# Performance work log

Measured on AMD Instinct MI355X. Metric: run time of the kernel, lower is better.

## Reference

```python
import jax, jax.numpy as jnp
import numpy as np

DIM_MODEL = 512
DIM_HEAD = 64


def setup_inputs() -> dict:
    key = jax.random.key(0)
    ks = jax.random.split(key, 7)
    B, S = 4, 4096
    x = jax.random.normal(ks[0], (B, S, DIM_MODEL), dtype=jnp.float32)
    mask = jnp.ones((B, 1, S), dtype=jnp.int32)
    # torch Linear init: U(-1/sqrt(fan_in), 1/sqrt(fan_in)); stored as (in, out) for x @ W
    bound = 1.0 / np.sqrt(DIM_MODEL)
    Wq = jax.random.uniform(ks[1], (DIM_MODEL, DIM_HEAD), minval=-bound, maxval=bound, dtype=jnp.float32)
    bq = jax.random.uniform(ks[2], (DIM_HEAD,), minval=-bound, maxval=bound, dtype=jnp.float32)
    Wk = jax.random.uniform(ks[3], (DIM_MODEL, DIM_HEAD), minval=-bound, maxval=bound, dtype=jnp.float32)
    bk = jax.random.uniform(ks[4], (DIM_HEAD,), minval=-bound, maxval=bound, dtype=jnp.float32)
    Wv = jax.random.uniform(ks[5], (DIM_MODEL, DIM_HEAD), minval=-bound, maxval=bound, dtype=jnp.float32)
    bv = jax.random.uniform(ks[6], (DIM_HEAD,), minval=-bound, maxval=bound, dtype=jnp.float32)
    return {"x": x, "mask": mask, "Wq": Wq, "bq": bq, "Wk": Wk, "bk": bk, "Wv": Wv, "bv": bv}


def reference(x, mask, Wq, bq, Wk, bk, Wv, bv):
    # single-head QKV projection
    q = x @ Wq + bq  # (B, S, Dh)
    k = x @ Wk + bk
    v = x @ Wv + bv
    dot_scale = jnp.sqrt(jnp.float32(DIM_HEAD))
    # explicit O(S^2) score matrix, softmax over keys
    scores = jnp.einsum("bqd,bkd->bqk", q, k) / dot_scale  # (B, S, S)
    attn = jax.nn.softmax(scores, axis=-1)
    # faithful to source: mask applied AFTER softmax with -inf fill
    attn = jnp.where(mask == 0, jnp.float32(-jnp.inf), attn)
    return jnp.einsum("bqk,bkd->bqd", attn, v)  # (B, S, Dh)
```

## Files before the change

kernel.cpp:

```cpp
#include <hip/hip_runtime.h>
#include <hip/hip_bf16.h>

typedef _Float16 half8v __attribute__((ext_vector_type(8)));
typedef _Float16 half4v __attribute__((ext_vector_type(4)));
typedef _Float16 half2v __attribute__((ext_vector_type(2)));
typedef __fp16   fp16x2 __attribute__((ext_vector_type(2)));
typedef __attribute__((ext_vector_type(4))) float floatx4;

#define LOG2E_OVER_8 0.18033688011112042f


__global__ __launch_bounds__(256) void wtrans_k(const float* __restrict__ Wq,
                                                const float* __restrict__ Wk,
                                                const float* __restrict__ Wv,
                                                _Float16* __restrict__ Wt) {
    int idx = blockIdx.x * 256 + threadIdx.x;
    int p = idx >> 15, rem = idx & 32767;
    int k = rem >> 6;
    int n = rem & 63;
    const float* W = (p == 0) ? Wq : ((p == 1) ? Wk : Wv);
    int ctg = p * 4 + (n >> 4), m = n & 15;
    int kc = k >> 5, quad = (k >> 3) & 3, j = k & 7;
    Wt[(((ctg << 4) + kc) * 64 + (quad << 4) + m) * 8 + j] = (_Float16)W[k * 64 + n];
}

#define XS_STRIDE 536
__global__ __launch_bounds__(256) void proj_k(const float* __restrict__ x,
                                              const _Float16* __restrict__ Wt,
                                              const float* __restrict__ bq,
                                              const float* __restrict__ bk,
                                              const float* __restrict__ bv,
                                              _Float16* __restrict__ Qh,
                                              _Float16* __restrict__ Kh,
                                              _Float16* __restrict__ Vh) {
    __shared__ _Float16 xs[16 * XS_STRIDE];

    int tid = threadIdx.x, l = tid & 63, wv = tid >> 6;
    int m = l & 15, quad = l >> 4;
    int row0 = blockIdx.x * 16;

#pragma unroll
    for (int i = 0; i < 8; i++) {
        int idx = tid + i * 256;
        int row = idx >> 7, c4 = idx & 127;
        float4 v = *(const float4*)(x + (row0 + row) * 512 + c4 * 4);
        union { half2v h[2]; uint2 u; } cv;
        cv.h[0][0] = (_Float16)v.x; cv.h[0][1] = (_Float16)v.y;
        cv.h[1][0] = (_Float16)v.z; cv.h[1][1] = (_Float16)v.w;
        *(uint2*)(xs + row * XS_STRIDE + c4 * 4) = cv.u;
    }
    __syncthreads();

    const _Float16* arow = xs + m * XS_STRIDE + quad * 8;

    floatx4 acc[3];
#pragma unroll
    for (int i = 0; i < 3; i++) acc[i] = (floatx4)(0.f);

#pragma unroll 4
    for (int kc = 0; kc < 16; kc++) {
        half8v a = *(const half8v*)(arow + kc * 32);
#pragma unroll
        for (int ct = 0; ct < 3; ct++) {
            int ctg = wv * 3 + ct;
            half8v b = *(const half8v*)(Wt + (((ctg << 4) + kc) * 64 + l) * 8);
            acc[ct] = __builtin_amdgcn_mfma_f32_16x16x32_f16(a, b, acc[ct], 0, 0, 0);
        }
    }

#pragma unroll
    for (int ct = 0; ct < 3; ct++) {
        int ctg = wv * 3 + ct;
        int col = ctg * 16 + m;
        float bias = (ctg < 4) ? bq[col] : ((ctg < 8) ? bk[col - 64] : bv[col - 128]);
        if (ctg < 8) {
            _Float16* dst = (ctg < 4) ? Qh : Kh;
            float scl = (ctg < 4) ? LOG2E_OVER_8 : 1.0f;
            int dd = (ctg & 3) * 16 + m;
            int c = dd >> 5, quadQ = (dd >> 3) & 3, j = dd & 7;
#pragma unroll
            for (int r = 0; r < 4; r++) {
                int row = row0 + quad * 4 + r;
                int chunk = ((row >> 4) << 1) + c;
                dst[(chunk * 64 + quadQ * 16 + (row & 15)) * 8 + j] =
                    (_Float16)((acc[ct][r] + bias) * scl);
            }
        } else {
            int dt = ctg - 8;
            int t64 = row0 >> 6, ktp = (row0 >> 5) & 1, half = (row0 >> 4) & 1;
            int chunk = t64 * 8 + dt * 2 + ktp;
            union { _Float16 h[4]; unsigned long long u; } pk;
#pragma unroll
            for (int r = 0; r < 4; r++) pk.h[r] = (_Float16)(acc[ct][r] + bias);
            *(unsigned long long*)(Vh + (chunk * 64 + quad * 16 + m) * 8 + half * 4) = pk.u;
        }
    }
}

__global__ __launch_bounds__(128) void attn_k(const _Float16* __restrict__ Qh,
                                              const _Float16* __restrict__ Kh,
                                              const _Float16* __restrict__ Vh,
                                              const int* __restrict__ mask,
                                              float* __restrict__ Np,
                                              float* __restrict__ Dp) {
    __shared__ __align__(16) uint4 buf[2][1024];

    int tid = threadIdx.x, l = tid & 63, wv = tid >> 6;
    int m = l & 15, quad = l >> 4;
    int bid = blockIdx.x;
    int qblk = bid >> 4, grp = bid & 15, os = grp >> 2, b = grp & 3;
    int q0 = qblk * 64 + wv * 32;

    const int* maskb = mask + b * 4096 + os * 1024;
    int az = 0;
#pragma unroll
    for (int i = 0; i < 16; i++) az |= (maskb[l + i * 64] == 0);
    const bool hasz = __any(az);

    int qt_g = (b * 4096 + q0) >> 4;
    half8v qf[2][2];
#pragma unroll
    for (int qt = 0; qt < 2; qt++)
#pragma unroll
        for (int c = 0; c < 2; c++)
            qf[qt][c] = *(const half8v*)(Qh + (((qt_g + qt) * 2 + c) * 64 + l) * 8);

    int tb0 = (b * 64 + os * 16) * 512;
    const uint4* gsrc = ((wv == 0) ? (const uint4*)Kh : (const uint4*)Vh) + tb0;

    floatx4 oacc[2][4];
#pragma unroll
    for (int qt = 0; qt < 2; qt++)
#pragma unroll
        for (int dt = 0; dt < 4; dt++) oacc[qt][dt] = (floatx4)(0.f);
    float dl[2] = {0.f, 0.f};

    typedef const __attribute__((address_space(1))) void gvoid;
    typedef __attribute__((address_space(3))) void lvoid;

#pragma unroll
    for (int j = 0; j < 8; j++)
        __builtin_amdgcn_global_load_lds(
            (gvoid*)(gsrc + j * 64 + l),
            (lvoid*)(&buf[0][(wv * 8 + j) * 64]), 16, 0, 0);

#pragma unroll 2
    for (int t = 0; t < 16; t++) {
        __syncthreads();
        if (t + 1 < 16) {
            const uint4* gs = gsrc + (t + 1) * 512;
            uint4* bn = &buf[(t + 1) & 1][0];
#pragma unroll
            for (int j = 0; j < 8; j++)
                __builtin_amdgcn_global_load_lds(
                    (gvoid*)(gs + j * 64 + l),
                    (lvoid*)(bn + (wv * 8 + j) * 64), 16, 0, 0);
        }
        const unsigned char* bk = (const unsigned char*)&buf[t & 1][0];
        const unsigned char* bv = bk + 8192;
        uint4 vv[4];
#pragma unroll
        for (int sub = 0; sub < 4; sub++) {
            half8v k0 = *(const half8v*)(bk + (sub * 2 + 0) * 1024 + l * 16);
            half8v k1 = *(const half8v*)(bk + (sub * 2 + 1) * 1024 + l * 16);
            if ((sub & 1) == 0) {
#pragma unroll
                for (int dt = 0; dt < 4; dt++)
                    vv[dt] = *(const uint4*)(bv + (dt * 2 + (sub >> 1)) * 1024 + l * 16);
            }
            half4v pb[2];
#pragma unroll
            for (int qt = 0; qt < 2; qt++) {
                floatx4 sf = (floatx4)(0.f);
                sf = __builtin_amdgcn_mfma_f32_16x16x32_f16(k0, qf[qt][0], sf, 0, 0, 0);
                sf = __builtin_amdgcn_mfma_f32_16x16x32_f16(k1, qf[qt][1], sf, 0, 0, 0);
                float p0 = exp2f(sf[0]), p1 = exp2f(sf[1]);
                float p2 = exp2f(sf[2]), p3 = exp2f(sf[3]);
                dl[qt] += (p0 + p1) + (p2 + p3);
                if (hasz) {
                    int kg = t * 64 + sub * 16 + quad * 4;
                    if (maskb[kg + 0] == 0) p0 = -__builtin_inff();
                    if (maskb[kg + 1] == 0) p1 = -__builtin_inff();
                    if (maskb[kg + 2] == 0) p2 = -__builtin_inff();
                    if (maskb[kg + 3] == 0) p3 = -__builtin_inff();
                }
                union { fp16x2 h[2]; half4v h4; } pu;
                pu.h[0] = __builtin_amdgcn_cvt_pkrtz(p0, p1);
                pu.h[1] = __builtin_amdgcn_cvt_pkrtz(p2, p3);
                pb[qt] = pu.h4;
            }
#pragma unroll
            for (int dt = 0; dt < 4; dt++) {
                union { uint4 u; half4v h[2]; } vc; vc.u = vv[dt];
                half4v va = vc.h[sub & 1];
                oacc[0][dt] = __builtin_amdgcn_mfma_f32_16x16x16f16(va, pb[0], oacc[0][dt], 0, 0, 0);
                oacc[1][dt] = __builtin_amdgcn_mfma_f32_16x16x16f16(va, pb[1], oacc[1][dt], 0, 0, 0);
            }
        }
    }

    __syncthreads();
    float* Tw = (float*)(&buf[0][0]) + wv * (16 * 68);
    int rowb = os * 16384 + b * 4096 + q0;
#pragma unroll
    for (int qt = 0; qt < 2; qt++) {
        float dqt = dl[qt];
        dqt += __shfl_xor(dqt, 16, 64);
        dqt += __shfl_xor(dqt, 32, 64);
        if (l < 16) Dp[rowb + qt * 16 + l] = dqt;
#pragma unroll
        for (int dt = 0; dt < 4; dt++)
#pragma unroll
            for (int r = 0; r < 4; r++)
                Tw[m * 68 + dt * 16 + quad * 4 + r] = oacc[qt][dt][r];
        __builtin_amdgcn_s_waitcnt(0);
#pragma unroll
        for (int g = 0; g < 4; g++) {
            int idx = g * 64 + l;
            int row = idx >> 4, c4 = (idx & 15) * 4;
            float4 v = *(const float4*)(Tw + row * 68 + c4);
            *(float4*)(Np + (rowb + qt * 16 + row) * 64 + c4) = v;
        }
        __builtin_amdgcn_s_waitcnt(0);
    }
}

__global__ __launch_bounds__(256) void combine_k(const float* __restrict__ Np,
                                                 const float* __restrict__ Dp,
                                                 float* __restrict__ out) {
    int g = blockIdx.x * 256 + threadIdx.x;
    int row = g >> 6;
    float nu = 0.f, d = 0.f;
#pragma unroll
    for (int sp = 0; sp < 4; sp++) {
        nu += Np[sp * 1048576 + g];
        d  += Dp[sp * 16384 + row];
    }
    out[g] = nu / d;
}

extern "C" void kernel_launch(void* const* d_in, const int* in_sizes, int n_in,
                              void* d_out, int out_size, void* d_ws, size_t ws_size,
                              hipStream_t stream) {
    const float* x  = (const float*)d_in[0];
    const int* mask = (const int*)d_in[1];
    const float* Wq = (const float*)d_in[2];
    const float* bq = (const float*)d_in[3];
    const float* Wk = (const float*)d_in[4];
    const float* bk = (const float*)d_in[5];
    const float* Wv = (const float*)d_in[6];
    const float* bv = (const float*)d_in[7];
    float* out = (float*)d_out;

    char* ws = (char*)d_ws;
    _Float16* Wt = (_Float16*)(ws);
    _Float16* Qh = (_Float16*)(ws + 0x40000);
    _Float16* Kh = (_Float16*)(ws + 0x240000);
    _Float16* Vh = (_Float16*)(ws + 0x440000);
    float*    Dp = (float*)(ws + 0x640000);
    float*    Np = (float*)(ws + 0x6C0000);

    wtrans_k<<<384, 256, 0, stream>>>(Wq, Wk, Wv, Wt);
    proj_k<<<1024, 256, 0, stream>>>(x, Wt, bq, bk, bv, Qh, Kh, Vh);
    attn_k<<<1024, 128, 0, stream>>>(Qh, Kh, Vh, mask, Np, Dp);
    combine_k<<<4096, 256, 0, stream>>>(Np, Dp, out);
}
```

Baseline: 144.8 us.

## Raise attention key-split from 4 to 8 and vectorize combine

The attention kernel now takes the key-split factor and tile count as runtime parameters. When workspace allows, it launches twice as many blocks, each covering half as many key tiles, to raise parallelism across the GPU's CUs. The combine kernel becomes float4-vectorized and loops over a variable number of splits. This trades more partial-sum traffic and combine work for better occupancy, and the loops are no longer fully unrolled because their bounds are runtime values.

Measured after the change: 154.2 us. +6.5%, slower.

```diff
diff --git a/kernel.cpp b/kernel.cpp
--- a/kernel.cpp
+++ b/kernel.cpp
@@ -102,19 +102,21 @@
                                               const _Float16* __restrict__ Vh,
                                               const int* __restrict__ mask,
                                               float* __restrict__ Np,
-                                              float* __restrict__ Dp) {
+                                              float* __restrict__ Dp,
+                                              int gshift, int nt) {
     __shared__ __align__(16) uint4 buf[2][1024];
 
     int tid = threadIdx.x, l = tid & 63, wv = tid >> 6;
     int m = l & 15, quad = l >> 4;
     int bid = blockIdx.x;
-    int qblk = bid >> 4, grp = bid & 15, os = grp >> 2, b = grp & 3;
+    int grp = bid & ((1 << gshift) - 1), qblk = bid >> gshift;
+    int os = grp >> 2, b = grp & 3;
     int q0 = qblk * 64 + wv * 32;
-
-    const int* maskb = mask + b * 4096 + os * 1024;
+    int kpb = nt * 64;
+
+    const int* maskb = mask + b * 4096 + os * kpb;
     int az = 0;
-#pragma unroll
-    for (int i = 0; i < 16; i++) az |= (maskb[l + i * 64] == 0);
+    for (int i = 0; i < nt; i++) az |= (maskb[l + i * 64] == 0);
     const bool hasz = __any(az);
 
     int qt_g = (b * 4096 + q0) >> 4;
@@ -125,7 +127,7 @@
         for (int c = 0; c < 2; c++)
             qf[qt][c] = *(const half8v*)(Qh + (((qt_g + qt) * 2 + c) * 64 + l) * 8);
 
-    int tb0 = (b * 64 + os * 16) * 512;
+    int tb0 = (b * 64 + os * nt) * 512;
     const uint4* gsrc = ((wv == 0) ? (const uint4*)Kh : (const uint4*)Vh) + tb0;
 
     floatx4 oacc[2][4];
@@ -145,9 +147,9 @@
             (lvoid*)(&buf[0][(wv * 8 + j) * 64]), 16, 0, 0);
 
 #pragma unroll 2
-    for (int t = 0; t < 16; t++) {
+    for (int t = 0; t < nt; t++) {
         __syncthreads();
-        if (t + 1 < 16) {
+        if (t + 1 < nt) {
             const uint4* gs = gsrc + (t + 1) * 512;
             uint4* bn = &buf[(t + 1) & 1][0];
 #pragma unroll
@@ -227,16 +229,19 @@
 
 __global__ __launch_bounds__(256) void combine_k(const float* __restrict__ Np,
                                                  const float* __restrict__ Dp,
-                                                 float* __restrict__ out) {
-    int g = blockIdx.x * 256 + threadIdx.x;
-    int row = g >> 6;
-    float nu = 0.f, d = 0.f;
-#pragma unroll
-    for (int sp = 0; sp < 4; sp++) {
-        nu += Np[sp * 1048576 + g];
-        d  += Dp[sp * 16384 + row];
-    }
-    out[g] = nu / d;
+                                                 float* __restrict__ out,
+                                                 int spl) {
+    int g4 = blockIdx.x * 256 + threadIdx.x;
+    int row = g4 >> 4;
+    float4 nu = make_float4(0.f, 0.f, 0.f, 0.f);
+    float d = 0.f;
+    for (int sp = 0; sp < spl; sp++) {
+        float4 v = ((const float4*)Np)[sp * 262144 + g4];
+        nu.x += v.x; nu.y += v.y; nu.z += v.z; nu.w += v.w;
+        d += Dp[sp * 16384 + row];
+    }
+    float inv = 1.0f / d;
+    ((float4*)out)[g4] = make_float4(nu.x * inv, nu.y * inv, nu.z * inv, nu.w * inv);
 }
 
 extern "C" void kernel_launch(void* const* d_in, const int* in_sizes, int n_in,
@@ -260,8 +265,13 @@
     float*    Dp = (float*)(ws + 0x640000);
     float*    Np = (float*)(ws + 0x6C0000);
 
+    size_t need8 = 0x6C0000 + (size_t)8 * 16384 * 64 * 4;
+    int spl = (ws_size >= need8) ? 8 : 4;
+    int gshift = (spl == 8) ? 5 : 4;
+    int nt = (spl == 8) ? 8 : 16;
+
     wtrans_k<<<384, 256, 0, stream>>>(Wq, Wk, Wv, Wt);
     proj_k<<<1024, 256, 0, stream>>>(x, Wt, bq, bk, bv, Qh, Kh, Vh);
-    attn_k<<<1024, 128, 0, stream>>>(Qh, Kh, Vh, mask, Np, Dp);
-    combine_k<<<4096, 256, 0, stream>>>(Np, Dp, out);
-}
+    attn_k<<<64 * 4 * spl, 128, 0, stream>>>(Qh, Kh, Vh, mask, Np, Dp, gshift, nt);
+    combine_k<<<1024, 256, 0, stream>>>(Np, Dp, out, spl);
+}
```
